# Kernel tuning notes

Measured on AMD Instinct MI355X. Metric: run time of the kernel, lower is better.

The kernel has to match this reference:

```python
import jax, jax.numpy as jnp
import numpy as np
import math

EPS = 1e-08
S = 64.0
MARGIN = 0.5
COS_M = math.cos(MARGIN)
SIN_M = math.sin(MARGIN)
B, D, C = 1024, 256, 200000


def setup_inputs() -> dict:
    key = jax.random.key(0)
    k1, k2, k3 = jax.random.split(key, 3)
    embeddings = jax.random.normal(k1, (B, D), dtype=jnp.float32)
    labels = jax.random.randint(k2, (B,), 0, C, dtype=jnp.int64)
    # xavier_uniform for prototypes [C, D]
    limit = math.sqrt(6.0 / (C + D))
    prototypes = jax.random.uniform(k3, (C, D), dtype=jnp.float32, minval=-limit, maxval=limit)
    return {"embeddings": embeddings, "labels": labels, "prototypes": prototypes}


def _l2norm(x):
    # torch F.normalize: x / max(||x||, 1e-12)
    n = jnp.sqrt(jnp.sum(x * x, axis=-1, keepdims=True))
    return x / jnp.maximum(n, 1e-12)


def reference(embeddings, labels, prototypes):
    e = _l2norm(embeddings)            # [B, D]
    p = _l2norm(prototypes)            # [C, D]
    cos_theta = jnp.einsum('bd,cd->bc', e, p)  # [B, C]
    sine_theta = jnp.clip(jnp.sqrt(jnp.maximum(1.0 - cos_theta * cos_theta, EPS)), EPS, 1.0 - EPS)
    phi = cos_theta * COS_M - sine_theta * SIN_M
    # apply margin only on the true-class column, then scale
    mask = jax.nn.one_hot(labels, C, dtype=cos_theta.dtype)
    logits = S * (mask * phi + (1.0 - mask) * cos_theta)
    logp = jax.nn.log_softmax(logits, axis=-1)
    loss = -jnp.mean(jnp.take_along_axis(logp, labels[:, None], axis=1))
    return loss
```

## Files before the change

kernel.cpp:

```cpp
#include <hip/hip_runtime.h>
#include <cstdint>
#include <cstddef>

#define D_DIM   256
#define B_ROWS  1024
#define C_CLS   200000
#define S_SC    64.0f
#define COS_M_F 0.87758256189037271612f
#define SIN_M_F 0.47942553860420300027f
#define EPS_F   1e-8f

#define CT 256
#define BT 128
#define NCT 782
#define CPAD (NCT * CT)
#define NPADROW (CPAD - C_CLS)
#define NBLK (NCT * 8)

typedef int   i32x4  __attribute__((ext_vector_type(4)));
typedef int   i32x8  __attribute__((ext_vector_type(8)));
typedef float f32x16 __attribute__((ext_vector_type(16)));

__global__ void k_norm_all8(const float* __restrict__ emb,
                            const float* __restrict__ proto,
                            unsigned char* __restrict__ ebf8,
                            unsigned char* __restrict__ pbf8) {
  int wid = threadIdx.x >> 6, lane = threadIdx.x & 63;
  int idx = (blockIdx.x << 2) + wid;
  const float* src;
  unsigned char* dst;
  if (idx < CPAD) {
    if (idx >= C_CLS) {
      *reinterpret_cast<unsigned int*>(pbf8 + (size_t)idx * D_DIM + lane * 4) = 0u;
      return;
    }
    src = proto + (size_t)idx * D_DIM;
    dst = pbf8 + (size_t)idx * D_DIM;
  } else {
    int row = idx - CPAD;
    src = emb + (size_t)row * D_DIM;
    dst = ebf8 + (size_t)row * D_DIM;
  }
  const float4 v = *reinterpret_cast<const float4*>(src + lane * 4);
  float ss = v.x * v.x + v.y * v.y + v.z * v.z + v.w * v.w;
#pragma unroll
  for (int m = 32; m >= 1; m >>= 1) ss += __shfl_xor(ss, m, 64);
  float inv = 1.0f / fmaxf(sqrtf(ss), 1e-12f);
  int packed = 0;
  packed = __builtin_amdgcn_cvt_pk_fp8_f32(v.x * inv, v.y * inv, packed, false);
  packed = __builtin_amdgcn_cvt_pk_fp8_f32(v.z * inv, v.w * inv, packed, true);
  *reinterpret_cast<int*>(dst + lane * 4) = packed;
}

__global__ __launch_bounds__(512, 4) void k_gemm_sw(
    const unsigned char* __restrict__ ebf8, const unsigned char* __restrict__ pbf8,
    float* __restrict__ sums) {
  __shared__ __align__(16) unsigned char Pls[CT * 256];
  __shared__ float bsum[BT];

  const int t = threadIdx.x;
  const int lane = t & 63;
  const int rsel = lane & 31;
  const int h = lane >> 5;
  const int wv = t >> 6;
  const int wc = wv >> 2;
  const int wb = wv & 3;

  int bid = (int)blockIdx.x;
  int w = (bid & 7) * NCT + (bid >> 3);
  const int ct = w >> 3;
  const int bt = w & 7;
  const int c0 = ct * CT;
  const int b0 = bt * BT;

#pragma unroll
  for (int j = 0; j < 8; ++j) {
    int G = j * 512 + t;
    int r = G >> 4, p = G & 15;
    int lg = p ^ (r & 15);
    const unsigned char* g = pbf8 + (size_t)(c0 + r) * D_DIM + lg * 16;
    __builtin_amdgcn_global_load_lds(
        (const __attribute__((address_space(1))) unsigned int*)(const void*)g,
        (__attribute__((address_space(3))) unsigned int*)(void*)(Pls + G * 16),
        16, 0, 0);
  }
  if (t < BT) bsum[t] = 0.0f;

  f32x16 acc[4];
#pragma unroll
  for (int mi = 0; mi < 4; ++mi)
#pragma unroll
    for (int e = 0; e < 16; ++e) acc[mi][e] = 0.0f;

  asm volatile("s_waitcnt vmcnt(0)" ::: "memory");
  __syncthreads();

  const unsigned char* ebase =
      ebf8 + (size_t)(b0 + wb * 32 + rsel) * D_DIM + h * 32;
#pragma unroll
  for (int ks = 0; ks < 4; ++ks) {
    i32x4 blo = *reinterpret_cast<const i32x4*>(ebase + ks * 64);
    i32x4 bhi = *reinterpret_cast<const i32x4*>(ebase + ks * 64 + 16);
    i32x8 bf = __builtin_shufflevector(blo, bhi, 0, 1, 2, 3, 4, 5, 6, 7);
    const int g = ks * 4 + h * 2;
#pragma unroll
    for (int mi = 0; mi < 4; ++mi) {
      int r = wc * 128 + mi * 32 + rsel;
      int p0 = g ^ (r & 15), p1 = (g + 1) ^ (r & 15);
      i32x4 lo = *reinterpret_cast<const i32x4*>(Pls + r * 256 + p0 * 16);
      i32x4 hi = *reinterpret_cast<const i32x4*>(Pls + r * 256 + p1 * 16);
      i32x8 af = __builtin_shufflevector(lo, hi, 0, 1, 2, 3, 4, 5, 6, 7);
      acc[mi] = __builtin_amdgcn_mfma_scale_f32_32x32x64_f8f6f4(
          af, bf, acc[mi], 0, 0,
          0, 0x7F7F7F7F, 0, 0x7F7F7F7F);
    }
  }

  float bp = 0.0f;
#pragma unroll
  for (int mi = 0; mi < 4; ++mi)
#pragma unroll
    for (int reg = 0; reg < 16; ++reg)
      bp += __expf(S_SC * acc[mi][reg]);
  bp += __shfl_xor(bp, 32, 64);
  if (lane < 32) atomicAdd(&bsum[wb * 32 + rsel], bp);
  __syncthreads();
  if (t < BT) atomicAdd(&sums[b0 + t], bsum[t]);
}

__device__ __forceinline__ float f8tof(unsigned char u) {
  int e = (u >> 3) & 15, m = u & 7;
  float mag = e ? ldexpf((float)(8 + m), e - 10) : ldexpf((float)m, -9);
  return (u & 0x80) ? -mag : mag;
}

__global__ void k_finalize(const unsigned char* __restrict__ ebf8,
                           const unsigned char* __restrict__ pbf8,
                           const int* __restrict__ labels,
                           const float* __restrict__ sums,
                           float* __restrict__ out) {
  __shared__ float part[4];
  int wid = threadIdx.x >> 6, lane = threadIdx.x & 63;
  int b = (blockIdx.x << 2) + wid;
  int lab = labels[b];
  const unsigned char* e = ebf8 + (size_t)b * D_DIM + lane * 4;
  const unsigned char* p = pbf8 + (size_t)lab * D_DIM + lane * 4;
  unsigned int eu = *reinterpret_cast<const unsigned int*>(e);
  unsigned int pu = *reinterpret_cast<const unsigned int*>(p);
  float dot = 0.0f;
#pragma unroll
  for (int i = 0; i < 4; ++i)
    dot += f8tof((eu >> (8 * i)) & 0xff) * f8tof((pu >> (8 * i)) & 0xff);
#pragma unroll
  for (int m = 32; m >= 1; m >>= 1) dot += __shfl_xor(dot, m, 64);
  if (lane == 0) {
    float cs = dot;
    float sn = sqrtf(fmaxf(1.0f - cs * cs, EPS_F));
    sn = fminf(fmaxf(sn, EPS_F), 1.0f - EPS_F);
    float phi = cs * COS_M_F - sn * SIN_M_F;
    float sp = S_SC * phi;
    float total = sums[b] - (float)NPADROW - __expf(S_SC * cs) + __expf(sp);
    part[wid] = logf(total) - sp;
  }
  __syncthreads();
  if (threadIdx.x == 0) {
    float s = part[0] + part[1] + part[2] + part[3];
    atomicAdd(out, s * (1.0f / (float)B_ROWS));
  }
}

extern "C" void kernel_launch(void* const* d_in, const int* in_sizes, int n_in,
                              void* d_out, int out_size, void* d_ws, size_t ws_size,
                              hipStream_t stream) {
  const float* emb    = (const float*)d_in[0];
  const int*   labels = (const int*)d_in[1];
  const float* proto  = (const float*)d_in[2];
  float* out = (float*)d_out;

  char* ws = (char*)d_ws;
  unsigned char* ebf8 = (unsigned char*)ws;
  float* sums = (float*)(ws + 262144);
  unsigned char* pbf8 = (unsigned char*)(ws + 2097152);

  hipMemsetAsync(sums, 0, B_ROWS * sizeof(float), stream);
  hipMemsetAsync(out, 0, sizeof(float), stream);

  k_norm_all8<<<(CPAD + B_ROWS) / 4, 256, 0, stream>>>(emb, proto, ebf8, pbf8);
  k_gemm_sw<<<NBLK, 512, 0, stream>>>(ebf8, pbf8, sums);
  k_finalize<<<B_ROWS / 4, 256, 0, stream>>>(ebf8, pbf8, labels, sums, out);
}
```

Baseline: 128.5 us.

## Keep prototype tiles in registers and loop over all batch rows per block

The GEMM kernel now assigns each block 256 classes and has each wave hold its 64 prototype rows in registers. It then loops over all 1024 embedding rows in 32-row steps, reading them directly from global memory and cache, and drops the LDS staging of prototype tiles. Per-row exp sums are collected in a shared array and flushed with one atomic per column per block, which cuts the atomic count and avoids rereading prototypes. The grid shrinks to 782 blocks of 4 waves, so each block carries a long serial loop and parallelism is lower. Embedding reloads rely on cache hits.

```diff
diff --git a/kernel.cpp b/kernel.cpp
--- a/kernel.cpp
+++ b/kernel.cpp
@@ -11,11 +11,9 @@
 #define EPS_F   1e-8f
 
 #define CT 256
-#define BT 128
-#define NCT 782
-#define CPAD (NCT * CT)
+#define NCB 782
+#define CPAD (NCB * CT)
 #define NPADROW (CPAD - C_CLS)
-#define NBLK (NCT * 8)
 
 typedef int   i32x4  __attribute__((ext_vector_type(4)));
 typedef int   i32x8  __attribute__((ext_vector_type(8)));
@@ -52,80 +50,74 @@
   *reinterpret_cast<int*>(dst + lane * 4) = packed;
 }
 
-__global__ __launch_bounds__(512, 4) void k_gemm_sw(
+__global__ __launch_bounds__(256, 3) void k_gemm_cls(
     const unsigned char* __restrict__ ebf8, const unsigned char* __restrict__ pbf8,
     float* __restrict__ sums) {
-  __shared__ __align__(16) unsigned char Pls[CT * 256];
-  __shared__ float bsum[BT];
+  __shared__ float bsum[4][B_ROWS];
 
   const int t = threadIdx.x;
   const int lane = t & 63;
   const int rsel = lane & 31;
   const int h = lane >> 5;
   const int wv = t >> 6;
-  const int wc = wv >> 2;
-  const int wb = wv & 3;
 
-  int bid = (int)blockIdx.x;
-  int w = (bid & 7) * NCT + (bid >> 3);
-  const int ct = w >> 3;
-  const int bt = w & 7;
-  const int c0 = ct * CT;
-  const int b0 = bt * BT;
+  const int c0 = (int)blockIdx.x * CT + wv * 64;
 
+  i32x8 af[2][4];
+  {
+    const unsigned char* ab = pbf8 + (size_t)(c0 + rsel) * D_DIM + h * 32;
 #pragma unroll
-  for (int j = 0; j < 8; ++j) {
-    int G = j * 512 + t;
-    int r = G >> 4, p = G & 15;
-    int lg = p ^ (r & 15);
-    const unsigned char* g = pbf8 + (size_t)(c0 + r) * D_DIM + lg * 16;
-    __builtin_amdgcn_global_load_lds(
-        (const __attribute__((address_space(1))) unsigned int*)(const void*)g,
-        (__attribute__((address_space(3))) unsigned int*)(void*)(Pls + G * 16),
-        16, 0, 0);
-  }
-  if (t < BT) bsum[t] = 0.0f;
-
-  f32x16 acc[4];
+    for (int mi = 0; mi < 2; ++mi)
 #pragma unroll
-  for (int mi = 0; mi < 4; ++mi)
-#pragma unroll
-    for (int e = 0; e < 16; ++e) acc[mi][e] = 0.0f;
-
-  asm volatile("s_waitcnt vmcnt(0)" ::: "memory");
-  __syncthreads();
-
-  const unsigned char* ebase =
-      ebf8 + (size_t)(b0 + wb * 32 + rsel) * D_DIM + h * 32;
-#pragma unroll
-  for (int ks = 0; ks < 4; ++ks) {
-    i32x4 blo = *reinterpret_cast<const i32x4*>(ebase + ks * 64);
-    i32x4 bhi = *reinterpret_cast<const i32x4*>(ebase + ks * 64 + 16);
-    i32x8 bf = __builtin_shufflevector(blo, bhi, 0, 1, 2, 3, 4, 5, 6, 7);
-    const int g = ks * 4 + h * 2;
-#pragma unroll
-    for (int mi = 0; mi < 4; ++mi) {
-      int r = wc * 128 + mi * 32 + rsel;
-      int p0 = g ^ (r & 15), p1 = (g + 1) ^ (r & 15);
-      i32x4 lo = *reinterpret_cast<const i32x4*>(Pls + r * 256 + p0 * 16);
-      i32x4 hi = *reinterpret_cast<const i32x4*>(Pls + r * 256 + p1 * 16);
-      i32x8 af = __builtin_shufflevector(lo, hi, 0, 1, 2, 3, 4, 5, 6, 7);
-      acc[mi] = __builtin_amdgcn_mfma_scale_f32_32x32x64_f8f6f4(
-          af, bf, acc[mi], 0, 0,
-          0, 0x7F7F7F7F, 0, 0x7F7F7F7F);
-    }
+      for (int ks = 0; ks < 4; ++ks) {
+        const unsigned char* p = ab + mi * (32 * D_DIM) + ks * 64;
+        i32x4 lo = *reinterpret_cast<const i32x4*>(p);
+        i32x4 hi = *reinterpret_cast<const i32x4*>(p + 16);
+        af[mi][ks] = __builtin_shufflevector(lo, hi, 0, 1, 2, 3, 4, 5, 6, 7);
+      }
   }
 
-  float bp = 0.0f;
+  const unsigned char* ebase = ebf8 + (size_t)rsel * D_DIM + h * 32;
+#pragma unroll 1
+  for (int s = 0; s < 32; ++s) {
+    const unsigned char* eb = ebase + (size_t)s * (32 * D_DIM);
+    i32x8 bf[4];
 #pragma unroll
-  for (int mi = 0; mi < 4; ++mi)
+    for (int ks = 0; ks < 4; ++ks) {
+      i32x4 lo = *reinterpret_cast<const i32x4*>(eb + ks * 64);
+      i32x4 hi = *reinterpret_cast<const i32x4*>(eb + ks * 64 + 16);
+      bf[ks] = __builtin_shufflevector(lo, hi, 0, 1, 2, 3, 4, 5, 6, 7);
+    }
+    f32x16 acc[2];
 #pragma unroll
-    for (int reg = 0; reg < 16; ++reg)
-      bp += __expf(S_SC * acc[mi][reg]);
-  bp += __shfl_xor(bp, 32, 64);
-  if (lane < 32) atomicAdd(&bsum[wb * 32 + rsel], bp);
+    for (int mi = 0; mi < 2; ++mi)
+#pragma unroll
+      for (int e = 0; e < 16; ++e) acc[mi][e] = 0.0f;
+#pragma unroll
+    for (int ks = 0; ks < 4; ++ks) {
+#pragma unroll
+      for (int mi = 0; mi < 2; ++mi)
+        acc[mi] = __builtin_amdgcn_mfma_scale_f32_32x32x64_f8f6f4(
+            af[mi][ks], bf[ks], acc[mi], 0, 0,
+            0, 0x7F7F7F7F, 0, 0x7F7F7F7F);
+    }
+    float bp = 0.0f;
+#pragma unroll
+    for (int mi = 0; mi < 2; ++mi)
+#pragma unroll
+      for (int e = 0; e < 16; ++e)
+        bp += __expf(S_SC * acc[mi][e]);
+    bp += __shfl_xor(bp, 32, 64);
+    if (h == 0) bsum[wv][s * 32 + rsel] = bp;
+  }
+
   __syncthreads();
-  if (t < BT) atomicAdd(&sums[b0 + t], bsum[t]);
+#pragma unroll
+  for (int j = 0; j < 4; ++j) {
+    int col = t + j * 256;
+    float v = bsum[0][col] + bsum[1][col] + bsum[2][col] + bsum[3][col];
+    atomicAdd(&sums[col], v);
+  }
 }
 
 __device__ __forceinline__ float f8tof(unsigned char u) {
@@ -186,6 +178,6 @@
   hipMemsetAsync(out, 0, sizeof(float), stream);
 
   k_norm_all8<<<(CPAD + B_ROWS) / 4, 256, 0, stream>>>(emb, proto, ebf8, pbf8);
-  k_gemm_sw<<<NBLK, 512, 0, stream>>>(ebf8, pbf8, sums);
+  k_gemm_cls<<<NCB, 256, 0, stream>>>(ebf8, pbf8, sums);
   k_finalize<<<B_ROWS / 4, 256, 0, stream>>>(ebf8, pbf8, labels, sums, out);
 }
```

Result: slower. 175.5 us (+36.6%).

## Enlarge batch tile to 256 rows per block and fold memsets into norm kernel

Applied to the files above, without the earlier changes.

Each GEMM block now covers 256 embedding rows instead of 128, halving the number of blocks. That halves how often each prototype tile is staged into LDS, so prototype global traffic drops. Waves loop over four 32-row embedding sub-tiles, each with two accumulators, which lowers register pressure per iteration but makes each block run serially longer. The zeroing of the sums and output buffers moves into the normalization kernel, removing two memset launches.

```diff
diff --git a/kernel.cpp b/kernel.cpp
--- a/kernel.cpp
+++ b/kernel.cpp
@@ -11,11 +11,12 @@
 #define EPS_F   1e-8f
 
 #define CT 256
-#define BT 128
 #define NCT 782
 #define CPAD (NCT * CT)
 #define NPADROW (CPAD - C_CLS)
-#define NBLK (NCT * 8)
+#define BT 256
+#define NBT 4
+#define NBLK (NCT * NBT)
 
 typedef int   i32x4  __attribute__((ext_vector_type(4)));
 typedef int   i32x8  __attribute__((ext_vector_type(8)));
@@ -24,7 +25,9 @@
 __global__ void k_norm_all8(const float* __restrict__ emb,
                             const float* __restrict__ proto,
                             unsigned char* __restrict__ ebf8,
-                            unsigned char* __restrict__ pbf8) {
+                            unsigned char* __restrict__ pbf8,
+                            float* __restrict__ sums,
+                            float* __restrict__ out) {
   int wid = threadIdx.x >> 6, lane = threadIdx.x & 63;
   int idx = (blockIdx.x << 2) + wid;
   const float* src;
@@ -38,6 +41,8 @@
     dst = pbf8 + (size_t)idx * D_DIM;
   } else {
     int row = idx - CPAD;
+    if (lane == 0) sums[row] = 0.0f;
+    if (idx == CPAD && lane == 1) *out = 0.0f;
     src = emb + (size_t)row * D_DIM;
     dst = ebf8 + (size_t)row * D_DIM;
   }
@@ -52,7 +57,7 @@
   *reinterpret_cast<int*>(dst + lane * 4) = packed;
 }
 
-__global__ __launch_bounds__(512, 4) void k_gemm_sw(
+__global__ __launch_bounds__(512, 4) void k_gemm_sw2(
     const unsigned char* __restrict__ ebf8, const unsigned char* __restrict__ pbf8,
     float* __restrict__ sums) {
   __shared__ __align__(16) unsigned char Pls[CT * 256];
@@ -63,13 +68,13 @@
   const int rsel = lane & 31;
   const int h = lane >> 5;
   const int wv = t >> 6;
-  const int wc = wv >> 2;
-  const int wb = wv & 3;
+  const int wc = wv >> 1;
+  const int wb = wv & 1;
 
   int bid = (int)blockIdx.x;
-  int w = (bid & 7) * NCT + (bid >> 3);
-  const int ct = w >> 3;
-  const int bt = w & 7;
+  int w = (bid & 7) * (NBLK / 8) + (bid >> 3);
+  const int ct = w >> 2;
+  const int bt = w & 3;
   const int c0 = ct * CT;
   const int b0 = bt * BT;
 
@@ -85,45 +90,51 @@
         16, 0, 0);
   }
   if (t < BT) bsum[t] = 0.0f;
-
-  f32x16 acc[4];
-#pragma unroll
-  for (int mi = 0; mi < 4; ++mi)
-#pragma unroll
-    for (int e = 0; e < 16; ++e) acc[mi][e] = 0.0f;
-
   asm volatile("s_waitcnt vmcnt(0)" ::: "memory");
   __syncthreads();
 
   const unsigned char* ebase =
-      ebf8 + (size_t)(b0 + wb * 32 + rsel) * D_DIM + h * 32;
-#pragma unroll
-  for (int ks = 0; ks < 4; ++ks) {
-    i32x4 blo = *reinterpret_cast<const i32x4*>(ebase + ks * 64);
-    i32x4 bhi = *reinterpret_cast<const i32x4*>(ebase + ks * 64 + 16);
-    i32x8 bf = __builtin_shufflevector(blo, bhi, 0, 1, 2, 3, 4, 5, 6, 7);
-    const int g = ks * 4 + h * 2;
-#pragma unroll
-    for (int mi = 0; mi < 4; ++mi) {
-      int r = wc * 128 + mi * 32 + rsel;
-      int p0 = g ^ (r & 15), p1 = (g + 1) ^ (r & 15);
-      i32x4 lo = *reinterpret_cast<const i32x4*>(Pls + r * 256 + p0 * 16);
-      i32x4 hi = *reinterpret_cast<const i32x4*>(Pls + r * 256 + p1 * 16);
-      i32x8 af = __builtin_shufflevector(lo, hi, 0, 1, 2, 3, 4, 5, 6, 7);
-      acc[mi] = __builtin_amdgcn_mfma_scale_f32_32x32x64_f8f6f4(
-          af, bf, acc[mi], 0, 0,
-          0, 0x7F7F7F7F, 0, 0x7F7F7F7F);
+      ebf8 + (size_t)(b0 + wb * 128 + rsel) * D_DIM + h * 32;
+#pragma unroll
+  for (int u = 0; u < 4; ++u) {
+    const unsigned char* eb = ebase + (size_t)u * (32 * D_DIM);
+    i32x8 bf[4];
+#pragma unroll
+    for (int ks = 0; ks < 4; ++ks) {
+      i32x4 lo = *reinterpret_cast<const i32x4*>(eb + ks * 64);
+      i32x4 hi = *reinterpret_cast<const i32x4*>(eb + ks * 64 + 16);
+      bf[ks] = __builtin_shufflevector(lo, hi, 0, 1, 2, 3, 4, 5, 6, 7);
     }
-  }
-
-  float bp = 0.0f;
-#pragma unroll
-  for (int mi = 0; mi < 4; ++mi)
-#pragma unroll
-    for (int reg = 0; reg < 16; ++reg)
-      bp += __expf(S_SC * acc[mi][reg]);
-  bp += __shfl_xor(bp, 32, 64);
-  if (lane < 32) atomicAdd(&bsum[wb * 32 + rsel], bp);
+    f32x16 acc[2];
+#pragma unroll
+    for (int mi = 0; mi < 2; ++mi)
+#pragma unroll
+      for (int e = 0; e < 16; ++e) acc[mi][e] = 0.0f;
+#pragma unroll
+    for (int ks = 0; ks < 4; ++ks) {
+      const int g = ks * 4 + h * 2;
+#pragma unroll
+      for (int mi = 0; mi < 2; ++mi) {
+        int ra = wc * 64 + mi * 32 + rsel;
+        int p0 = g ^ (ra & 15), p1 = (g + 1) ^ (ra & 15);
+        i32x4 lo = *reinterpret_cast<const i32x4*>(Pls + ra * 256 + p0 * 16);
+        i32x4 hi = *reinterpret_cast<const i32x4*>(Pls + ra * 256 + p1 * 16);
+        i32x8 af = __builtin_shufflevector(lo, hi, 0, 1, 2, 3, 4, 5, 6, 7);
+        acc[mi] = __builtin_amdgcn_mfma_scale_f32_32x32x64_f8f6f4(
+            af, bf[ks], acc[mi], 0, 0,
+            0, 0x7F7F7F7F, 0, 0x7F7F7F7F);
+      }
+    }
+    float bp = 0.0f;
+#pragma unroll
+    for (int mi = 0; mi < 2; ++mi)
+#pragma unroll
+      for (int e = 0; e < 16; ++e)
+        bp += __expf(S_SC * acc[mi][e]);
+    bp += __shfl_xor(bp, 32, 64);
+    if (h == 0) atomicAdd(&bsum[wb * 128 + u * 32 + rsel], bp);
+  }
+
   __syncthreads();
   if (t < BT) atomicAdd(&sums[b0 + t], bsum[t]);
 }
@@ -182,10 +193,8 @@
   float* sums = (float*)(ws + 262144);
   unsigned char* pbf8 = (unsigned char*)(ws + 2097152);
 
-  hipMemsetAsync(sums, 0, B_ROWS * sizeof(float), stream);
-  hipMemsetAsync(out, 0, sizeof(float), stream);
-
-  k_norm_all8<<<(CPAD + B_ROWS) / 4, 256, 0, stream>>>(emb, proto, ebf8, pbf8);
-  k_gemm_sw<<<NBLK, 512, 0, stream>>>(ebf8, pbf8, sums);
+  k_norm_all8<<<(CPAD + B_ROWS) / 4, 256, 0, stream>>>(emb, proto, ebf8, pbf8,
+                                                       sums, out);
+  k_gemm_sw2<<<NBLK, 512, 0, stream>>>(ebf8, pbf8, sums);
   k_finalize<<<B_ROWS / 4, 256, 0, stream>>>(ebf8, pbf8, labels, sums, out);
 }
```

New measurement: 152.4 us. 1.19x slower.
